# Kernel optimization log

Measured on AMD Instinct MI355X. Metric: run time of the kernel, lower is better.

The kernel has to match this reference:

```python
import jax, jax.numpy as jnp
import numpy as np

VOCAB = 8000
IN_FEATURES = 256
P = 8  # half-window; neighbor_num = 2*P
B, L = 16, 2048


def setup_inputs() -> dict:
    key = jax.random.key(0)
    k1, k2, k3, k4 = jax.random.split(key, 4)
    input_ids = jax.random.randint(k1, (B, L), 0, VOCAB, dtype=jnp.int32)
    # node_embedding: default torch init (normal), padding_idx=0 row zeroed
    node_emb = jax.random.normal(k2, (VOCAB, IN_FEATURES), dtype=jnp.float32)
    node_emb = node_emb.at[0].set(0.0)
    # edge_weight and node_weight re-initialized with xavier_uniform (padding row NOT re-zeroed, matching source)
    lim_e = float(np.sqrt(6.0 / (VOCAB * VOCAB + 1 + 1)))
    edge_w = jax.random.uniform(k3, (VOCAB * VOCAB + 1, 1), minval=-lim_e, maxval=lim_e, dtype=jnp.float32)
    lim_n = float(np.sqrt(6.0 / (VOCAB + 1)))
    node_w = jax.random.uniform(k4, (VOCAB, 1), minval=-lim_n, maxval=lim_n, dtype=jnp.float32)
    return {"input_ids": input_ids, "node_emb": node_emb, "edge_w": edge_w, "node_w": node_w}


def _neighbors(input_ids):
    # vectorized sliding-window neighbor construction (replaces the python loop)
    b, l = input_ids.shape
    xp = jnp.pad(input_ids, ((0, 0), (P, P)))  # (B, L+2P)
    offsets = jnp.concatenate([jnp.arange(P), jnp.arange(P + 1, 2 * P + 1)])  # (2P,)
    idx = jnp.arange(l)[:, None] + offsets[None, :]  # (L, 2P)
    NX = xp[:, idx]  # (B, L, 2P)
    EW = input_ids[:, :, None].astype(jnp.int32) * VOCAB + NX
    EW = jnp.where(NX == 0, 0, EW)
    return NX, EW


def reference(input_ids, node_emb, edge_w, node_w):
    NX, EW = _neighbors(input_ids)
    Ra = node_emb[NX]              # (B, L, 2P, D) gather
    Ean = edge_w[EW]               # (B, L, 2P, 1) gather
    Mn = jnp.max(Ra * Ean, axis=2)  # (B, L, D) max over neighbors
    Rn = node_emb[input_ids]       # (B, L, D)
    Nn = node_w[input_ids]         # (B, L, 1)
    y = (1.0 - Nn) * Mn + Nn * Rn   # gated sum
    return y.sum(axis=1)           # (B, D)
```

## Files before the change

kernel.cpp:

```cpp
#include <hip/hip_runtime.h>


#define VOCAB 8000
#define FDIM  256
#define PNB   8
#define NK    16
#define BB    16
#define LL    2048
#define CHUNK 32

__global__ void gnn_zero_out(float* __restrict__ out) {
    out[blockIdx.x * 256 + threadIdx.x] = 0.0f;
}

__global__ __launch_bounds__(256) void gnn_kernel(
    const int*   __restrict__ ids,
    const float* __restrict__ emb,
    const float* __restrict__ edge_w,
    const float* __restrict__ node_w,
    float*       __restrict__ out)
{
    __shared__ int   s_nbr[CHUNK][NK];
    __shared__ float s_ew [CHUNK][NK];
    __shared__ int   s_c  [CHUNK];
    __shared__ float s_nw [CHUNK];
    __shared__ float s_red[4][FDIM];

    const int b   = blockIdx.y;
    const int l0  = blockIdx.x * CHUNK;
    const int tid = threadIdx.x;
    const int* idrow = ids + b * LL;

    for (int i = tid; i < CHUNK * NK; i += 256) {
        const int ll = i >> 4;
        const int k  = i & (NK - 1);
        const int l  = l0 + ll;
        const int d  = (k < PNB) ? (k - PNB) : (k - PNB + 1);
        const int li = l + d;
        int n = (li >= 0 && li < LL) ? idrow[li] : 0;
        n = (n < 0) ? 0 : ((n >= VOCAB) ? (VOCAB - 1) : n);
        int c = idrow[l];
        c = (c < 0) ? 0 : ((c >= VOCAB) ? (VOCAB - 1) : c);
        const long long ei = (n == 0) ? 0LL : (long long)c * VOCAB + n;
        s_nbr[ll][k] = n;
        s_ew [ll][k] = edge_w[ei];
    }
    if (tid < CHUNK) {
        int c = idrow[l0 + tid];
        c = (c < 0) ? 0 : ((c >= VOCAB) ? (VOCAB - 1) : c);
        s_c [tid] = c;
        s_nw[tid] = node_w[c];
    }
    __syncthreads();

    const int wave = tid >> 6;
    const int lane = tid & 63;
    const int f0   = lane << 2;

    float4 acc = make_float4(0.f, 0.f, 0.f, 0.f);
    for (int ll = wave; ll < CHUNK; ll += 4) {
        const int   c  = s_c [ll];
        const float nw = s_nw[ll];
        float4 m = make_float4(-INFINITY, -INFINITY, -INFINITY, -INFINITY);
        #pragma unroll
        for (int k = 0; k < NK; ++k) {
            const int   n = s_nbr[ll][k];
            const float e = s_ew [ll][k];
            const float4 r = *(const float4*)(emb + (size_t)n * FDIM + f0);
            m.x = fmaxf(m.x, e * r.x);
            m.y = fmaxf(m.y, e * r.y);
            m.z = fmaxf(m.z, e * r.z);
            m.w = fmaxf(m.w, e * r.w);
        }
        const float4 rc = *(const float4*)(emb + (size_t)c * FDIM + f0);
        const float w1 = 1.0f - nw;
        acc.x += w1 * m.x + nw * rc.x;
        acc.y += w1 * m.y + nw * rc.y;
        acc.z += w1 * m.z + nw * rc.z;
        acc.w += w1 * m.w + nw * rc.w;
    }

    ((float4*)s_red[wave])[lane] = acc;
    __syncthreads();

    const float s = s_red[0][tid] + s_red[1][tid] + s_red[2][tid] + s_red[3][tid];
    atomicAdd(out + b * FDIM + tid, s);
}

extern "C" void kernel_launch(void* const* d_in, const int* in_sizes, int n_in,
                              void* d_out, int out_size, void* d_ws, size_t ws_size,
                              hipStream_t stream) {
    const int*   ids    = nullptr;
    const float* emb    = nullptr;
    const float* edge_w = nullptr;
    const float* node_w = nullptr;
    for (int i = 0; i < n_in; ++i) {
        const long long sz = in_sizes[i];
        if      (sz == (long long)BB * LL)            ids    = (const int*)  d_in[i];
        else if (sz == (long long)VOCAB * FDIM)       emb    = (const float*)d_in[i];
        else if (sz == (long long)VOCAB * VOCAB + 1)  edge_w = (const float*)d_in[i];
        else if (sz == (long long)VOCAB)              node_w = (const float*)d_in[i];
    }
    float* out = (float*)d_out;

    gnn_zero_out<<<dim3(out_size / 256), dim3(256), 0, stream>>>(out);

    dim3 grid(LL / CHUNK, BB);
    gnn_kernel<<<grid, 256, 0, stream>>>(ids, emb, edge_w, node_w, out);
}
```

Before: 343.7 us.

## Stage sliding-window embedding rows in shared memory to reuse across neighbors

Loads the window of CHUNK+2P token embeddings once into shared memory per block and reads all neighbor and center rows from LDS, instead of gathering each of the 16 neighbor rows from global memory for every position. CHUNK drops from 32 to 16, so the grid doubles and the halo overhead per block grows. Each row's index is computed from the window position rather than stored. About 32 KB of LDS per block may limit occupancy, and the halo rows are loaded redundantly by adjacent blocks.

```diff
diff --git a/kernel.cpp b/kernel.cpp
--- a/kernel.cpp
+++ b/kernel.cpp
@@ -7,7 +7,8 @@
 #define NK    16
 #define BB    16
 #define LL    2048
-#define CHUNK 32
+#define CHUNK 16
+#define WIN   (CHUNK + 2*PNB)
 
 __global__ void gnn_zero_out(float* __restrict__ out) {
     out[blockIdx.x * 256 + threadIdx.x] = 0.0f;
@@ -20,9 +21,9 @@
     const float* __restrict__ node_w,
     float*       __restrict__ out)
 {
-    __shared__ int   s_nbr[CHUNK][NK];
+    __shared__ float s_emb[WIN][FDIM];
     __shared__ float s_ew [CHUNK][NK];
-    __shared__ int   s_c  [CHUNK];
+    __shared__ int   s_tok[WIN];
     __shared__ float s_nw [CHUNK];
     __shared__ float s_red[4][FDIM];
 
@@ -31,25 +32,32 @@
     const int tid = threadIdx.x;
     const int* idrow = ids + b * LL;
 
-    for (int i = tid; i < CHUNK * NK; i += 256) {
-        const int ll = i >> 4;
-        const int k  = i & (NK - 1);
-        const int l  = l0 + ll;
-        const int d  = (k < PNB) ? (k - PNB) : (k - PNB + 1);
-        const int li = l + d;
-        int n = (li >= 0 && li < LL) ? idrow[li] : 0;
-        n = (n < 0) ? 0 : ((n >= VOCAB) ? (VOCAB - 1) : n);
-        int c = idrow[l];
-        c = (c < 0) ? 0 : ((c >= VOCAB) ? (VOCAB - 1) : c);
+    if (tid < WIN) {
+        const int p = l0 - PNB + tid;
+        int t = (p >= 0 && p < LL) ? idrow[p] : 0;
+        t = (t < 0) ? 0 : ((t >= VOCAB) ? (VOCAB - 1) : t);
+        s_tok[tid] = t;
+    }
+    __syncthreads();
+
+    {
+        const int ll = tid >> 4;
+        const int k  = tid & (NK - 1);
+        const int n  = s_tok[ll + k + (k >= PNB ? 1 : 0)];
+        const int c  = s_tok[ll + PNB];
         const long long ei = (n == 0) ? 0LL : (long long)c * VOCAB + n;
-        s_nbr[ll][k] = n;
-        s_ew [ll][k] = edge_w[ei];
+        s_ew[ll][k] = edge_w[ei];
+        if (tid < CHUNK) s_nw[tid] = node_w[s_tok[tid + PNB]];
     }
-    if (tid < CHUNK) {
-        int c = idrow[l0 + tid];
-        c = (c < 0) ? 0 : ((c >= VOCAB) ? (VOCAB - 1) : c);
-        s_c [tid] = c;
-        s_nw[tid] = node_w[c];
+    {
+        #pragma unroll
+        for (int j = 0; j < 8; ++j) {
+            const int i    = tid + 256 * j;
+            const int row  = i >> 6;
+            const int col4 = (i & 63) << 2;
+            const float4 v = *(const float4*)(emb + (size_t)s_tok[row] * FDIM + col4);
+            *(float4*)&s_emb[row][col4] = v;
+        }
     }
     __syncthreads();
 
@@ -58,21 +66,22 @@
     const int f0   = lane << 2;
 
     float4 acc = make_float4(0.f, 0.f, 0.f, 0.f);
-    for (int ll = wave; ll < CHUNK; ll += 4) {
-        const int   c  = s_c [ll];
+    #pragma unroll
+    for (int q = 0; q < CHUNK / 4; ++q) {
+        const int ll = (wave << 2) + q;
         const float nw = s_nw[ll];
         float4 m = make_float4(-INFINITY, -INFINITY, -INFINITY, -INFINITY);
         #pragma unroll
         for (int k = 0; k < NK; ++k) {
-            const int   n = s_nbr[ll][k];
-            const float e = s_ew [ll][k];
-            const float4 r = *(const float4*)(emb + (size_t)n * FDIM + f0);
+            const int widx = ll + k + (k >= PNB ? 1 : 0);
+            const float  e = s_ew[ll][k];
+            const float4 r = *(const float4*)&s_emb[widx][f0];
             m.x = fmaxf(m.x, e * r.x);
             m.y = fmaxf(m.y, e * r.y);
             m.z = fmaxf(m.z, e * r.z);
             m.w = fmaxf(m.w, e * r.w);
         }
-        const float4 rc = *(const float4*)(emb + (size_t)c * FDIM + f0);
+        const float4 rc = *(const float4*)&s_emb[ll + PNB][f0];
         const float w1 = 1.0f - nw;
         acc.x += w1 * m.x + nw * rc.x;
         acc.y += w1 * m.y + nw * rc.y;
```

New measurement: 322.3 us. 1.07x faster.
